# Optimization experiments

Hardware: AMD Instinct MI355X
Metric: run time of the kernel (lower is better)

## Reference

```python
import jax, jax.numpy as jnp
from jax import lax
import numpy as np

BLANK = 0
PAD = 1
LABEL_SMOOTHING = 0.1
CE_SCALE = 1.0
TEMPERATURE = 1.0

B, T, U1, D, V = 8, 128, 33, 512, 4096  # U1 = U + 1


def setup_inputs() -> dict:
    key = jax.random.key(0)
    k0, k1, k2, k3, k4 = jax.random.split(key, 5)
    x = jax.random.normal(k0, (B, T, U1, D), dtype=jnp.float32)
    weight = jax.random.normal(k1, (V, D), dtype=jnp.float32) * 0.02
    bias = jnp.zeros((V,), dtype=jnp.float32)
    src_lengths = jax.random.randint(k2, (B,), T // 2, T + 1, dtype=jnp.int32)
    tgt_lengths = jax.random.randint(k3, (B,), U1 // 2, U1, dtype=jnp.int32)
    targets = jax.random.randint(k4, (B, U1 - 1), 2, V, dtype=jnp.int32)
    pos = jnp.arange(U1 - 1, dtype=jnp.int32)
    targets = jnp.where(pos[None, :] < tgt_lengths[:, None], targets, PAD)
    return {'x': x, 'weight': weight, 'bias': bias, 'targets': targets,
            'src_lengths': src_lengths, 'tgt_lengths': tgt_lengths}


def _rnnt_neglogp(blank_lp, emit_lp, src_lengths, tgt_lengths):
    """RNN-T forward DP. blank_lp: (B,T,U1) log P(blank); emit_lp: (B,T,U) log P(y_u).
    Returns per-utterance negative log-likelihood, shape (B,)."""
    Bn, Tn, U1n = blank_lp.shape
    # alpha at t=0: can only emit labels -> prefix-sum of emit log-probs
    alpha0 = jnp.concatenate(
        [jnp.zeros((Bn, 1), blank_lp.dtype), jnp.cumsum(emit_lp[:, 0, :], axis=1)], axis=1)

    def t_step(alpha_prev, xs):
        blank_prev, emit_t = xs  # (B,U1), (B,U)
        a = alpha_prev + blank_prev  # blank transition from t-1
        def u_step(c, xu):
            a_u, e_prev = xu  # each (B,)
            c = jnp.logaddexp(a_u, c + e_prev)  # emit transition from u-1 at same t
            return c, c
        _, rest = lax.scan(u_step, a[:, 0], (a[:, 1:].T, emit_t.T))  # rest: (U,B)
        alpha_t = jnp.concatenate([a[:, :1], rest.T], axis=1)
        return alpha_t, alpha_t

    xs = (jnp.swapaxes(blank_lp[:, :-1], 0, 1), jnp.swapaxes(emit_lp[:, 1:], 0, 1))
    _, alphas_rest = lax.scan(t_step, alpha0, xs)  # (T-1,B,U1)
    alphas = jnp.concatenate([alpha0[None], alphas_rest], axis=0)  # (T,B,U1)
    bidx = jnp.arange(Bn)
    alpha_last_t = alphas[src_lengths - 1, bidx]  # (B,U1)
    a_fin = jnp.take_along_axis(alpha_last_t, tgt_lengths[:, None], axis=1)[:, 0]
    b_fin = blank_lp[bidx, src_lengths - 1, tgt_lengths]  # final blank emission
    return -(a_fin + b_fin)


def reference(x, weight, bias, targets, src_lengths, tgt_lengths):
    Vn = weight.shape[0]
    # joint logits over full lattice: (B,T,U1,V)
    logits = (jnp.einsum('btud,vd->btuv', x, weight) + bias).astype(jnp.float32)
    lp = jax.nn.log_softmax(logits / TEMPERATURE, axis=-1)
    blank_lp = lp[..., BLANK]  # (B,T,U1)
    emit_lp = jnp.take_along_axis(lp[:, :, :-1, :], targets[:, None, :, None].astype(jnp.int32), axis=3)[..., 0]  # (B,T,U)
    loss_prob = jnp.sum(_rnnt_neglogp(blank_lp, emit_lp, src_lengths, tgt_lengths))
    loss_delay = jnp.zeros((), jnp.float32)  # delay_func == 'zero'
    # label-smoothed CE on last valid encoder frame
    last_h = jnp.take_along_axis(x, (src_lengths - 1)[:, None, None, None], axis=1)[:, 0]  # (B,U1,D)
    last_h = last_h[:, :-1]  # (B,U,D)
    ce_logits = (jnp.einsum('bud,vd->buv', last_h, weight) + bias).astype(jnp.float32)
    lprobs = jax.nn.log_softmax(ce_logits, axis=-1)
    nll = -jnp.take_along_axis(lprobs, targets[..., None], axis=-1)[..., 0]  # (B,U)
    smooth = -jnp.sum(lprobs, axis=-1)
    mask = (targets != PAD).astype(lprobs.dtype)
    eps_i = LABEL_SMOOTHING / (Vn - 1)
    loss_smoothed = jnp.sum(((1.0 - LABEL_SMOOTHING - eps_i) * nll + eps_i * smooth) * mask)
    total = loss_prob + loss_delay + CE_SCALE * loss_smoothed
    return total
```

## Files before the change

kernel.cpp:

```cpp
#include <hip/hip_runtime.h>
#include <hip/hip_bf16.h>
#include <math.h>
#include <stdint.h>

#define B_ 8
#define T_ 128
#define U1_ 33
#define D_ 512
#define V_ 4096
#define M_ (B_*T_*U1_)

#define BLANK_ 0
#define PAD_ 1

#define TM 128
#define TN 128
#define BKB 128
#define NK (D_/BKB)
#define GN (V_/TN)

typedef __attribute__((ext_vector_type(4))) float fvec4;
typedef __attribute__((ext_vector_type(8))) int   i8v;
typedef __attribute__((ext_vector_type(4))) int   i4v;

#define SCALE_A 0x7F7F7F7Fu
#define SCALE_B 0x79797979u

__device__ __forceinline__ void load_lds16(const uint8_t* g, uint8_t* l) {
    __builtin_amdgcn_global_load_lds(
        (const __attribute__((address_space(1))) unsigned int*)g,
        (__attribute__((address_space(3))) unsigned int*)l, 16, 0, 0);
}

__device__ __forceinline__ unsigned pack4_fp8(fvec4 v) {
    int r = __builtin_amdgcn_cvt_pk_fp8_f32(v.x, v.y, 0, false);
    r = __builtin_amdgcn_cvt_pk_fp8_f32(v.z, v.w, r, true);
    return (unsigned)r;
}

__global__ void convert_kernel(const float* __restrict__ x, const float* __restrict__ w,
                               uint8_t* __restrict__ xf8, uint8_t* __restrict__ wf8)
{
    int i = blockIdx.x * 256 + threadIdx.x;
    int stride = gridDim.x * 256;
    const int nx = (M_ * D_) / 16;
    const int nw = (V_ * D_) / 16;
    for (int j = i; j < nx; j += stride) {
        const fvec4* p = (const fvec4*)x + (size_t)j * 4;
        uint4 o = { pack4_fp8(p[0]), pack4_fp8(p[1]), pack4_fp8(p[2]), pack4_fp8(p[3]) };
        ((uint4*)xf8)[j] = o;
    }
    for (int j = i; j < nw; j += stride) {
        const fvec4* p = (const fvec4*)w + (size_t)j * 4;
        fvec4 v0 = p[0]*64.0f, v1 = p[1]*64.0f, v2 = p[2]*64.0f, v3 = p[3]*64.0f;
        uint4 o = { pack4_fp8(v0), pack4_fp8(v1), pack4_fp8(v2), pack4_fp8(v3) };
        ((uint4*)wf8)[j] = o;
    }
}

__global__ void wsum_kernel(const float* __restrict__ w, const float* __restrict__ bias,
                            float* __restrict__ wsum)
{
    const int t = threadIdx.x;
    const int v0 = blockIdx.x * 128;
    float s0 = 0.0f, s1 = 0.0f;
    for (int v = 0; v < 128; v++) {
        s0 += w[(size_t)(v0 + v) * D_ + t];
        s1 += w[(size_t)(v0 + v) * D_ + t + 256];
    }
    atomicAdd(&wsum[t], s0);
    atomicAdd(&wsum[t + 256], s1);
    if (blockIdx.x == 0) {
        float b = 0.0f;
        for (int v = t; v < V_; v += 256) b += bias[v];
        atomicAdd(&wsum[D_], b);
    }
}

__global__ __launch_bounds__(256, 2)
void gemm_fused(const uint8_t* __restrict__ xf8, const uint8_t* __restrict__ wf8,
                const float* __restrict__ bias, const int* __restrict__ targets,
                float* __restrict__ partial_e,
                float* __restrict__ blank_z, float* __restrict__ emit_z)
{
    __shared__ __align__(16) uint8_t As[2][TM * BKB];
    __shared__ __align__(16) uint8_t Bs[2][TN * BKB];
    __shared__ float ps[TM];
    __shared__ int tgt_s[TM];

    const int tid  = threadIdx.x;
    const int lane = tid & 63;
    const int wid  = tid >> 6;
    const int m0   = blockIdx.x * TM;
    const int n0   = blockIdx.y * TN;

    const int srow = wid * 32 + (lane >> 3);
    const int schk = (lane & 7) ^ ((lane >> 3) & 7);
    const uint8_t* agp = xf8 + (size_t)(m0 + srow) * D_ + schk * 16;
    const uint8_t* bgp = wf8 + (size_t)(n0 + srow) * D_ + schk * 16;

    fvec4 acc[4][4];
#pragma unroll
    for (int i = 0; i < 4; i++)
#pragma unroll
        for (int j = 0; j < 4; j++) acc[i][j] = (fvec4)0.0f;

    const int wrow = (wid >> 1) * 64;
    const int wcol = (wid & 1) * 64;
    const int m15  = lane & 15;
    const int quad = lane >> 4;

    auto stage = [&](int buf, int ks) {
        const uint8_t* ag = agp + ks * BKB;
        const uint8_t* bg = bgp + ks * BKB;
#pragma unroll
        for (int j = 0; j < 4; j++) {
            load_lds16(ag + j * 8 * D_, &As[buf][(wid * 32 + j * 8) * BKB]);
            load_lds16(bg + j * 8 * D_, &Bs[buf][(wid * 32 + j * 8) * BKB]);
        }
    };

    stage(0, 0);
    if (tid < TM) {
        ps[tid] = 0.0f;
        int row = m0 + tid;
        int u = row % U1_;
        int b = row / (T_ * U1_);
        tgt_s[tid] = (u < U1_ - 1) ? targets[b * (U1_ - 1) + u] : -1;
    }
    __syncthreads();

    const int e   = m15 & 7;
    const int c0b = (((quad << 1) ^ e) << 4);

    for (int ks = 0; ks < NK; ks++) {
        const int cur = ks & 1;
        if (ks + 1 < NK) {
            stage(cur ^ 1, ks + 1);
            asm volatile("s_waitcnt vmcnt(8)" ::: "memory");
        } else {
            asm volatile("s_waitcnt vmcnt(0)" ::: "memory");
        }
        __builtin_amdgcn_s_barrier();

        i8v fa[4], fb[4];
#pragma unroll
        for (int mi = 0; mi < 4; mi++) {
            int base = (wrow + mi * 16 + m15) << 7;
            union { i4v h[2]; i8v w; } u;
            u.h[0] = *(const i4v*)&As[cur][base + c0b];
            u.h[1] = *(const i4v*)&As[cur][base + (c0b ^ 16)];
            fa[mi] = u.w;
        }
#pragma unroll
        for (int ni = 0; ni < 4; ni++) {
            int base = (wcol + ni * 16 + m15) << 7;
            union { i4v h[2]; i8v w; } u;
            u.h[0] = *(const i4v*)&Bs[cur][base + c0b];
            u.h[1] = *(const i4v*)&Bs[cur][base + (c0b ^ 16)];
            fb[ni] = u.w;
        }
#pragma unroll
        for (int mi = 0; mi < 4; mi++)
#pragma unroll
            for (int ni = 0; ni < 4; ni++)
                acc[mi][ni] = __builtin_amdgcn_mfma_scale_f32_16x16x128_f8f6f4(
                                  fa[mi], fb[ni], acc[mi][ni],
                                  0, 0,
                                  0, SCALE_A, 0, SCALE_B);
        __builtin_amdgcn_s_barrier();
    }

    float bv[4];
#pragma unroll
    for (int ni = 0; ni < 4; ni++) bv[ni] = bias[n0 + wcol + ni * 16 + m15];

    const bool blank_lane = (blockIdx.y == 0) && (wcol == 0) && (m15 == 0);

#pragma unroll
    for (int mi = 0; mi < 4; mi++) {
#pragma unroll
        for (int r = 0; r < 4; r++) {
            const int irow = wrow + mi * 16 + quad * 4 + r;
            float se = 0.0f;
#pragma unroll
            for (int ni = 0; ni < 4; ni++) {
                float z = acc[mi][ni][r] + bv[ni];
                se += __expf(z);
                int c = n0 + wcol + ni * 16 + m15;
                if (tgt_s[irow] == c) emit_z[m0 + irow] = z;
            }
            if (blank_lane) blank_z[m0 + irow] = acc[mi][0][r] + bv[0];
            se += __shfl_xor(se, 1, 64);
            se += __shfl_xor(se, 2, 64);
            se += __shfl_xor(se, 4, 64);
            se += __shfl_xor(se, 8, 64);
            if (m15 == 0) atomicAdd(&ps[irow], se);
        }
    }
    __syncthreads();
    if (tid < TM) {
        partial_e[(size_t)blockIdx.y * M_ + m0 + tid] = ps[tid];
    }
}

__global__ void lse_combine(const float* __restrict__ partial_e,
                            const float* __restrict__ emit_z, const int* __restrict__ targets,
                            const int* __restrict__ src_lengths,
                            const float* __restrict__ x, const float* __restrict__ wsum,
                            float* __restrict__ lse, float* __restrict__ out)
{
    int r = blockIdx.x * 256 + threadIdx.x;
    float se = 0.0f;
#pragma unroll
    for (int j = 0; j < GN; j++) se += partial_e[(size_t)j * M_ + r];
    float l = __logf(se);
    lse[r] = l;

    int b   = r / (T_ * U1_);
    int rem = r % (T_ * U1_);
    int t   = rem / U1_;
    int u   = rem % U1_;
    if (u < U1_ - 1 && t == src_lengths[b] - 1) {
        int tgt = targets[b * (U1_ - 1) + u];
        if (tgt != PAD_) {
            float sz = wsum[D_];
            const fvec4* xr = (const fvec4*)(x + (size_t)r * D_);
            const fvec4* ws = (const fvec4*)wsum;
#pragma unroll 4
            for (int d = 0; d < D_ / 4; d++) {
                fvec4 a = xr[d], wv = ws[d];
                sz += a.x * wv.x + a.y * wv.y + a.z * wv.z + a.w * wv.w;
            }
            float nll    = l - emit_z[r];
            float smooth = (float)V_ * l - sz;
            const float eps_i = 0.1f / (float)(V_ - 1);
            atomicAdd(out, (1.0f - 0.1f - eps_i) * nll + eps_i * smooth);
        }
    }
}

__global__ __launch_bounds__(256)
void dp_kernel(const float* __restrict__ blank_z, const float* __restrict__ emit_z,
               const float* __restrict__ lse, const int* __restrict__ src_lengths,
               const int* __restrict__ tgt_lengths, float* __restrict__ out)
{
    __shared__ float blp[T_ * U1_];
    __shared__ float elp[T_ * U1_];
    const int tid = threadIdx.x;
    const int b = blockIdx.x;
    for (int i = tid; i < T_ * U1_; i += 256) {
        int g = b * T_ * U1_ + i;
        float l = lse[g];
        blp[i] = blank_z[g] - l;
        elp[i] = emit_z[g] - l;
    }
    __syncthreads();
    if (tid >= 64) return;

    const int u = tid;
    const int ua = (u < U1_) ? u : U1_ - 1;
    const int sl = src_lengths[b], tl = tgt_lengths[b];

    float val = 0.0f;
    float afin = 0.0f;

    for (int d = 1; d <= (T_ - 1) + (U1_ - 1); d++) {
        int t = d - u;
        int tb = t - 1; tb = tb < 0 ? 0 : (tb > T_ - 1 ? T_ - 1 : tb);
        int tc = t < 0 ? 0 : (t > T_ - 1 ? T_ - 1 : t);
        float blv = blp[tb * U1_ + ua];
        float elv = elp[tc * U1_ + (ua > 0 ? ua - 1 : 0)];
        float up = __shfl_up(val, 1, 64);
        bool valid = (u < U1_) && (t >= 0) && (t < T_);
        if (valid) {
            if (t == 0) {
                val = up + elv;
            } else if (u == 0) {
                val = val + blv;
            } else {
                float a1 = val + blv;
                float a2 = up + elv;
                float mx = fmaxf(a1, a2), mn = fminf(a1, a2);
                val = mx + log1pf(__expf(mn - mx));
            }
            if (t == sl - 1 && u == tl) afin = val;
        }
    }
#pragma unroll
    for (int off = 1; off < 64; off <<= 1) afin += __shfl_xor(afin, off, 64);
    if (u == 0) {
        float bfin = blp[(sl - 1) * U1_ + tl];
        atomicAdd(out, -(afin + bfin));
    }
}

extern "C" void kernel_launch(void* const* d_in, const int* in_sizes, int n_in,
                              void* d_out, int out_size, void* d_ws, size_t ws_size,
                              hipStream_t stream)
{
    const float* x           = (const float*)d_in[0];
    const float* w           = (const float*)d_in[1];
    const float* bias        = (const float*)d_in[2];
    const int*   targets     = (const int*)d_in[3];
    const int*   src_lengths = (const int*)d_in[4];
    const int*   tgt_lengths = (const int*)d_in[5];
    float* out = (float*)d_out;

    char* p = (char*)d_ws;
    uint8_t* xf8 = (uint8_t*)p;     p += (size_t)M_ * D_;
    uint8_t* wf8 = (uint8_t*)p;     p += (size_t)V_ * D_;
    float* partial_e = (float*)p;   p += (size_t)GN * M_ * sizeof(float);
    float* lse       = (float*)p;   p += (size_t)M_ * sizeof(float);
    float* blank_z   = (float*)p;   p += (size_t)M_ * sizeof(float);
    float* emit_z    = (float*)p;   p += (size_t)M_ * sizeof(float);
    float* wsum      = (float*)p;   p += (size_t)(D_ + 4) * sizeof(float);

    hipMemsetAsync(out, 0, sizeof(float), stream);
    hipMemsetAsync(wsum, 0, (D_ + 4) * sizeof(float), stream);

    convert_kernel<<<1536, 256, 0, stream>>>(x, w, xf8, wf8);
    wsum_kernel<<<32, 256, 0, stream>>>(w, bias, wsum);
    gemm_fused<<<dim3(M_/TM, V_/TN), 256, 0, stream>>>(xf8, wf8, bias, targets,
                                                       partial_e, blank_z, emit_z);
    lse_combine<<<M_/256, 256, 0, stream>>>(partial_e, emit_z, targets,
                                            src_lengths, x, wsum, lse, out);
    dp_kernel<<<B_, 256, 0, stream>>>(blank_z, emit_z, lse, src_lengths, tgt_lengths, out);
}
```

Measured before the change: 451.9 us.

## Fuse wsum into convert, merge LSE combine into DP, swizzle GEMM tiles by XCD

The separate weight-sum kernel is folded into the conversion kernel. The LSE reduction and the label-smoothed CE term move into the DP kernel, which drops a launch and the lse buffer. The GEMM maps blocks to tiles grouped per XCD for better L2 locality, and the K loop now synchronises with __syncthreads instead of manual vmcnt waits. The risk is that the DP kernel runs only 8 blocks, so reducing all 32 partial sums per row there may be slow and latency-bound.

```diff
diff --git a/kernel.cpp b/kernel.cpp
--- a/kernel.cpp
+++ b/kernel.cpp
@@ -39,7 +39,9 @@
 }
 
 __global__ void convert_kernel(const float* __restrict__ x, const float* __restrict__ w,
-                               uint8_t* __restrict__ xf8, uint8_t* __restrict__ wf8)
+                               const float* __restrict__ bias,
+                               uint8_t* __restrict__ xf8, uint8_t* __restrict__ wf8,
+                               float* __restrict__ wsum)
 {
     int i = blockIdx.x * 256 + threadIdx.x;
     int stride = gridDim.x * 256;
@@ -56,24 +58,21 @@
         uint4 o = { pack4_fp8(v0), pack4_fp8(v1), pack4_fp8(v2), pack4_fp8(v3) };
         ((uint4*)wf8)[j] = o;
     }
-}
-
-__global__ void wsum_kernel(const float* __restrict__ w, const float* __restrict__ bias,
-                            float* __restrict__ wsum)
-{
-    const int t = threadIdx.x;
-    const int v0 = blockIdx.x * 128;
-    float s0 = 0.0f, s1 = 0.0f;
-    for (int v = 0; v < 128; v++) {
-        s0 += w[(size_t)(v0 + v) * D_ + t];
-        s1 += w[(size_t)(v0 + v) * D_ + t + 256];
-    }
-    atomicAdd(&wsum[t], s0);
-    atomicAdd(&wsum[t + 256], s1);
-    if (blockIdx.x == 0) {
-        float b = 0.0f;
-        for (int v = t; v < V_; v += 256) b += bias[v];
-        atomicAdd(&wsum[D_], b);
+    if (blockIdx.x < 32) {
+        const int t = threadIdx.x;
+        const int v0 = blockIdx.x * 128;
+        float s0 = 0.0f, s1 = 0.0f;
+        for (int v = 0; v < 128; v++) {
+            s0 += w[(size_t)(v0 + v) * D_ + t];
+            s1 += w[(size_t)(v0 + v) * D_ + t + 256];
+        }
+        atomicAdd(&wsum[t], s0);
+        atomicAdd(&wsum[t + 256], s1);
+        if (blockIdx.x == 0) {
+            float bsum = 0.0f;
+            for (int v = t; v < V_; v += 256) bsum += bias[v];
+            atomicAdd(&wsum[D_], bsum);
+        }
     }
 }
 
@@ -91,8 +90,14 @@
     const int tid  = threadIdx.x;
     const int lane = tid & 63;
     const int wid  = tid >> 6;
-    const int m0   = blockIdx.x * TM;
-    const int n0   = blockIdx.y * TN;
+
+    const int fid = blockIdx.y * gridDim.x + blockIdx.x;
+    const int xcd = fid & 7;
+    const int idx = fid >> 3;
+    const int mt  = xcd * 33 + (idx >> 5);
+    const int nt  = idx & 31;
+    const int m0  = mt * TM;
+    const int n0  = nt * TN;
 
     const int srow = wid * 32 + (lane >> 3);
     const int schk = (lane & 7) ^ ((lane >> 3) & 7);
@@ -121,6 +126,43 @@
     };
 
     stage(0, 0);
+    __syncthreads();
+
+    const int e   = m15 & 7;
+    const int c0b = (((quad << 1) ^ e) << 4);
+
+    for (int ks = 0; ks < NK; ks++) {
+        const int cur = ks & 1;
+        if (ks + 1 < NK) stage(cur ^ 1, ks + 1);
+
+        i8v fa[4], fb[4];
+#pragma unroll
+        for (int mi = 0; mi < 4; mi++) {
+            int base = (wrow + mi * 16 + m15) << 7;
+            union { i4v h[2]; i8v w; } u;
+            u.h[0] = *(const i4v*)&As[cur][base + c0b];
+            u.h[1] = *(const i4v*)&As[cur][base + (c0b ^ 16)];
+            fa[mi] = u.w;
+        }
+#pragma unroll
+        for (int ni = 0; ni < 4; ni++) {
+            int base = (wcol + ni * 16 + m15) << 7;
+            union { i4v h[2]; i8v w; } u;
+            u.h[0] = *(const i4v*)&Bs[cur][base + c0b];
+            u.h[1] = *(const i4v*)&Bs[cur][base + (c0b ^ 16)];
+            fb[ni] = u.w;
+        }
+#pragma unroll
+        for (int mi = 0; mi < 4; mi++)
+#pragma unroll
+            for (int ni = 0; ni < 4; ni++)
+                acc[mi][ni] = __builtin_amdgcn_mfma_scale_f32_16x16x128_f8f6f4(
+                                  fa[mi], fb[ni], acc[mi][ni],
+                                  0, 0,
+                                  0, SCALE_A, 0, SCALE_B);
+        __syncthreads();
+    }
+
     if (tid < TM) {
         ps[tid] = 0.0f;
         int row = m0 + tid;
@@ -130,52 +172,11 @@
     }
     __syncthreads();
 
-    const int e   = m15 & 7;
-    const int c0b = (((quad << 1) ^ e) << 4);
-
-    for (int ks = 0; ks < NK; ks++) {
-        const int cur = ks & 1;
-        if (ks + 1 < NK) {
-            stage(cur ^ 1, ks + 1);
-            asm volatile("s_waitcnt vmcnt(8)" ::: "memory");
-        } else {
-            asm volatile("s_waitcnt vmcnt(0)" ::: "memory");
-        }
-        __builtin_amdgcn_s_barrier();
-
-        i8v fa[4], fb[4];
-#pragma unroll
-        for (int mi = 0; mi < 4; mi++) {
-            int base = (wrow + mi * 16 + m15) << 7;
-            union { i4v h[2]; i8v w; } u;
-            u.h[0] = *(const i4v*)&As[cur][base + c0b];
-            u.h[1] = *(const i4v*)&As[cur][base + (c0b ^ 16)];
-            fa[mi] = u.w;
-        }
-#pragma unroll
-        for (int ni = 0; ni < 4; ni++) {
-            int base = (wcol + ni * 16 + m15) << 7;
-            union { i4v h[2]; i8v w; } u;
-            u.h[0] = *(const i4v*)&Bs[cur][base + c0b];
-            u.h[1] = *(const i4v*)&Bs[cur][base + (c0b ^ 16)];
-            fb[ni] = u.w;
-        }
-#pragma unroll
-        for (int mi = 0; mi < 4; mi++)
-#pragma unroll
-            for (int ni = 0; ni < 4; ni++)
-                acc[mi][ni] = __builtin_amdgcn_mfma_scale_f32_16x16x128_f8f6f4(
-                                  fa[mi], fb[ni], acc[mi][ni],
-                                  0, 0,
-                                  0, SCALE_A, 0, SCALE_B);
-        __builtin_amdgcn_s_barrier();
-    }
-
     float bv[4];
 #pragma unroll
     for (int ni = 0; ni < 4; ni++) bv[ni] = bias[n0 + wcol + ni * 16 + m15];
 
-    const bool blank_lane = (blockIdx.y == 0) && (wcol == 0) && (m15 == 0);
+    const bool blank_lane = (nt == 0) && (wcol == 0) && (m15 == 0);
 
 #pragma unroll
     for (int mi = 0; mi < 4; mi++) {
@@ -200,67 +201,65 @@
     }
     __syncthreads();
     if (tid < TM) {
-        partial_e[(size_t)blockIdx.y * M_ + m0 + tid] = ps[tid];
-    }
-}
-
-__global__ void lse_combine(const float* __restrict__ partial_e,
-                            const float* __restrict__ emit_z, const int* __restrict__ targets,
-                            const int* __restrict__ src_lengths,
-                            const float* __restrict__ x, const float* __restrict__ wsum,
-                            float* __restrict__ lse, float* __restrict__ out)
-{
-    int r = blockIdx.x * 256 + threadIdx.x;
-    float se = 0.0f;
-#pragma unroll
-    for (int j = 0; j < GN; j++) se += partial_e[(size_t)j * M_ + r];
-    float l = __logf(se);
-    lse[r] = l;
-
-    int b   = r / (T_ * U1_);
-    int rem = r % (T_ * U1_);
-    int t   = rem / U1_;
-    int u   = rem % U1_;
-    if (u < U1_ - 1 && t == src_lengths[b] - 1) {
-        int tgt = targets[b * (U1_ - 1) + u];
-        if (tgt != PAD_) {
-            float sz = wsum[D_];
-            const fvec4* xr = (const fvec4*)(x + (size_t)r * D_);
-            const fvec4* ws = (const fvec4*)wsum;
-#pragma unroll 4
-            for (int d = 0; d < D_ / 4; d++) {
-                fvec4 a = xr[d], wv = ws[d];
-                sz += a.x * wv.x + a.y * wv.y + a.z * wv.z + a.w * wv.w;
-            }
-            float nll    = l - emit_z[r];
-            float smooth = (float)V_ * l - sz;
-            const float eps_i = 0.1f / (float)(V_ - 1);
-            atomicAdd(out, (1.0f - 0.1f - eps_i) * nll + eps_i * smooth);
-        }
+        partial_e[(size_t)nt * M_ + m0 + tid] = ps[tid];
     }
 }
 
 __global__ __launch_bounds__(256)
-void dp_kernel(const float* __restrict__ blank_z, const float* __restrict__ emit_z,
-               const float* __restrict__ lse, const int* __restrict__ src_lengths,
-               const int* __restrict__ tgt_lengths, float* __restrict__ out)
+void dp_kernel(const float* __restrict__ partial_e,
+               const float* __restrict__ blank_z, const float* __restrict__ emit_z,
+               const int* __restrict__ targets,
+               const int* __restrict__ src_lengths, const int* __restrict__ tgt_lengths,
+               const float* __restrict__ x, const float* __restrict__ wsum,
+               float* __restrict__ out)
 {
     __shared__ float blp[T_ * U1_];
     __shared__ float elp[T_ * U1_];
     const int tid = threadIdx.x;
     const int b = blockIdx.x;
+    const int sl = src_lengths[b], tl = tgt_lengths[b];
+
     for (int i = tid; i < T_ * U1_; i += 256) {
         int g = b * T_ * U1_ + i;
-        float l = lse[g];
+        float se = 0.0f;
+#pragma unroll
+        for (int j = 0; j < GN; j++) se += partial_e[(size_t)j * M_ + g];
+        float l = __logf(se);
         blp[i] = blank_z[g] - l;
         elp[i] = emit_z[g] - l;
     }
     __syncthreads();
-    if (tid >= 64) return;
+
+    if (tid >= 64) {
+        if (tid < 64 + (U1_ - 1)) {
+            int u = tid - 64;
+            int tgt = targets[b * (U1_ - 1) + u];
+            if (tgt != PAD_) {
+                int i = (sl - 1) * U1_ + u;
+                int g = b * T_ * U1_ + i;
+                float se = 0.0f;
+#pragma unroll
+                for (int j = 0; j < GN; j++) se += partial_e[(size_t)j * M_ + g];
+                float l = __logf(se);
+                float sz = wsum[D_];
+                const fvec4* xr = (const fvec4*)(x + (size_t)g * D_);
+                const fvec4* ws = (const fvec4*)wsum;
+#pragma unroll 4
+                for (int d = 0; d < D_ / 4; d++) {
+                    fvec4 a = xr[d], wv = ws[d];
+                    sz += a.x * wv.x + a.y * wv.y + a.z * wv.z + a.w * wv.w;
+                }
+                float nll    = l - emit_z[g];
+                float smooth = (float)V_ * l - sz;
+                const float eps_i = 0.1f / (float)(V_ - 1);
+                atomicAdd(out, (1.0f - 0.1f - eps_i) * nll + eps_i * smooth);
+            }
+        }
+        return;
+    }
 
     const int u = tid;
     const int ua = (u < U1_) ? u : U1_ - 1;
-    const int sl = src_lengths[b], tl = tgt_lengths[b];
 
     float val = 0.0f;
     float afin = 0.0f;
@@ -311,7 +310,6 @@
     uint8_t* xf8 = (uint8_t*)p;     p += (size_t)M_ * D_;
     uint8_t* wf8 = (uint8_t*)p;     p += (size_t)V_ * D_;
     float* partial_e = (float*)p;   p += (size_t)GN * M_ * sizeof(float);
-    float* lse       = (float*)p;   p += (size_t)M_ * sizeof(float);
     float* blank_z   = (float*)p;   p += (size_t)M_ * sizeof(float);
     float* emit_z    = (float*)p;   p += (size_t)M_ * sizeof(float);
     float* wsum      = (float*)p;   p += (size_t)(D_ + 4) * sizeof(float);
@@ -319,11 +317,9 @@
     hipMemsetAsync(out, 0, sizeof(float), stream);
     hipMemsetAsync(wsum, 0, (D_ + 4) * sizeof(float), stream);
 
-    convert_kernel<<<1536, 256, 0, stream>>>(x, w, xf8, wf8);
-    wsum_kernel<<<32, 256, 0, stream>>>(w, bias, wsum);
+    convert_kernel<<<1536, 256, 0, stream>>>(x, w, bias, xf8, wf8, wsum);
     gemm_fused<<<dim3(M_/TM, V_/TN), 256, 0, stream>>>(xf8, wf8, bias, targets,
                                                        partial_e, blank_z, emit_z);
-    lse_combine<<<M_/256, 256, 0, stream>>>(partial_e, emit_z, targets,
-                                            src_lengths, x, wsum, lse, out);
-    dp_kernel<<<B_, 256, 0, stream>>>(blank_z, emit_z, lse, src_lengths, tgt_lengths, out);
-}
+    dp_kernel<<<B_, 256, 0, stream>>>(partial_e, blank_z, emit_z, targets,
+                                      src_lengths, tgt_lengths, x, wsum, out);
+}
```

Result: faster. 418.6 us (-7.4%).

## Fuse wsum into convert kernel, remap GEMM tiles per XCD, simplify k-loop sync

Applied to the files above, without the earlier changes.

Folds the weight column-sum kernel into the fp8 conversion kernel, saving one launch. Remaps GEMM block indices so each XCD (fid&7) works on a contiguous band of 33 M-tiles across all 32 N-tiles, aiming for better L2 reuse of the A rows. Moves the target/ps setup after the main loop and replaces the manual vmcnt waits with plain __syncthreads. The plain barriers may leave the async global_load_lds prefetch less well overlapped with compute, or unsynchronised if the compiler does not insert a vmcnt wait before the barrier.

```diff
diff --git a/kernel.cpp b/kernel.cpp
--- a/kernel.cpp
+++ b/kernel.cpp
@@ -39,7 +39,9 @@
 }
 
 __global__ void convert_kernel(const float* __restrict__ x, const float* __restrict__ w,
-                               uint8_t* __restrict__ xf8, uint8_t* __restrict__ wf8)
+                               const float* __restrict__ bias,
+                               uint8_t* __restrict__ xf8, uint8_t* __restrict__ wf8,
+                               float* __restrict__ wsum)
 {
     int i = blockIdx.x * 256 + threadIdx.x;
     int stride = gridDim.x * 256;
@@ -56,24 +58,21 @@
         uint4 o = { pack4_fp8(v0), pack4_fp8(v1), pack4_fp8(v2), pack4_fp8(v3) };
         ((uint4*)wf8)[j] = o;
     }
-}
-
-__global__ void wsum_kernel(const float* __restrict__ w, const float* __restrict__ bias,
-                            float* __restrict__ wsum)
-{
-    const int t = threadIdx.x;
-    const int v0 = blockIdx.x * 128;
-    float s0 = 0.0f, s1 = 0.0f;
-    for (int v = 0; v < 128; v++) {
-        s0 += w[(size_t)(v0 + v) * D_ + t];
-        s1 += w[(size_t)(v0 + v) * D_ + t + 256];
-    }
-    atomicAdd(&wsum[t], s0);
-    atomicAdd(&wsum[t + 256], s1);
-    if (blockIdx.x == 0) {
-        float b = 0.0f;
-        for (int v = t; v < V_; v += 256) b += bias[v];
-        atomicAdd(&wsum[D_], b);
+    if (blockIdx.x < 32) {
+        const int t = threadIdx.x;
+        const int v0 = blockIdx.x * 128;
+        float s0 = 0.0f, s1 = 0.0f;
+        for (int v = 0; v < 128; v++) {
+            s0 += w[(size_t)(v0 + v) * D_ + t];
+            s1 += w[(size_t)(v0 + v) * D_ + t + 256];
+        }
+        atomicAdd(&wsum[t], s0);
+        atomicAdd(&wsum[t + 256], s1);
+        if (blockIdx.x == 0) {
+            float bsum = 0.0f;
+            for (int v = t; v < V_; v += 256) bsum += bias[v];
+            atomicAdd(&wsum[D_], bsum);
+        }
     }
 }
 
@@ -91,8 +90,14 @@
     const int tid  = threadIdx.x;
     const int lane = tid & 63;
     const int wid  = tid >> 6;
-    const int m0   = blockIdx.x * TM;
-    const int n0   = blockIdx.y * TN;
+
+    const int fid = blockIdx.y * gridDim.x + blockIdx.x;
+    const int xcd = fid & 7;
+    const int idx = fid >> 3;
+    const int mt  = xcd * 33 + (idx >> 5);
+    const int nt  = idx & 31;
+    const int m0  = mt * TM;
+    const int n0  = nt * TN;
 
     const int srow = wid * 32 + (lane >> 3);
     const int schk = (lane & 7) ^ ((lane >> 3) & 7);
@@ -121,6 +126,43 @@
     };
 
     stage(0, 0);
+    __syncthreads();
+
+    const int e   = m15 & 7;
+    const int c0b = (((quad << 1) ^ e) << 4);
+
+    for (int ks = 0; ks < NK; ks++) {
+        const int cur = ks & 1;
+        if (ks + 1 < NK) stage(cur ^ 1, ks + 1);
+
+        i8v fa[4], fb[4];
+#pragma unroll
+        for (int mi = 0; mi < 4; mi++) {
+            int base = (wrow + mi * 16 + m15) << 7;
+            union { i4v h[2]; i8v w; } u;
+            u.h[0] = *(const i4v*)&As[cur][base + c0b];
+            u.h[1] = *(const i4v*)&As[cur][base + (c0b ^ 16)];
+            fa[mi] = u.w;
+        }
+#pragma unroll
+        for (int ni = 0; ni < 4; ni++) {
+            int base = (wcol + ni * 16 + m15) << 7;
+            union { i4v h[2]; i8v w; } u;
+            u.h[0] = *(const i4v*)&Bs[cur][base + c0b];
+            u.h[1] = *(const i4v*)&Bs[cur][base + (c0b ^ 16)];
+            fb[ni] = u.w;
+        }
+#pragma unroll
+        for (int mi = 0; mi < 4; mi++)
+#pragma unroll
+            for (int ni = 0; ni < 4; ni++)
+                acc[mi][ni] = __builtin_amdgcn_mfma_scale_f32_16x16x128_f8f6f4(
+                                  fa[mi], fb[ni], acc[mi][ni],
+                                  0, 0,
+                                  0, SCALE_A, 0, SCALE_B);
+        __syncthreads();
+    }
+
     if (tid < TM) {
         ps[tid] = 0.0f;
         int row = m0 + tid;
@@ -130,52 +172,11 @@
     }
     __syncthreads();
 
-    const int e   = m15 & 7;
-    const int c0b = (((quad << 1) ^ e) << 4);
-
-    for (int ks = 0; ks < NK; ks++) {
-        const int cur = ks & 1;
-        if (ks + 1 < NK) {
-            stage(cur ^ 1, ks + 1);
-            asm volatile("s_waitcnt vmcnt(8)" ::: "memory");
-        } else {
-            asm volatile("s_waitcnt vmcnt(0)" ::: "memory");
-        }
-        __builtin_amdgcn_s_barrier();
-
-        i8v fa[4], fb[4];
-#pragma unroll
-        for (int mi = 0; mi < 4; mi++) {
-            int base = (wrow + mi * 16 + m15) << 7;
-            union { i4v h[2]; i8v w; } u;
-            u.h[0] = *(const i4v*)&As[cur][base + c0b];
-            u.h[1] = *(const i4v*)&As[cur][base + (c0b ^ 16)];
-            fa[mi] = u.w;
-        }
-#pragma unroll
-        for (int ni = 0; ni < 4; ni++) {
-            int base = (wcol + ni * 16 + m15) << 7;
-            union { i4v h[2]; i8v w; } u;
-            u.h[0] = *(const i4v*)&Bs[cur][base + c0b];
-            u.h[1] = *(const i4v*)&Bs[cur][base + (c0b ^ 16)];
-            fb[ni] = u.w;
-        }
-#pragma unroll
-        for (int mi = 0; mi < 4; mi++)
-#pragma unroll
-            for (int ni = 0; ni < 4; ni++)
-                acc[mi][ni] = __builtin_amdgcn_mfma_scale_f32_16x16x128_f8f6f4(
-                                  fa[mi], fb[ni], acc[mi][ni],
-                                  0, 0,
-                                  0, SCALE_A, 0, SCALE_B);
-        __builtin_amdgcn_s_barrier();
-    }
-
     float bv[4];
 #pragma unroll
     for (int ni = 0; ni < 4; ni++) bv[ni] = bias[n0 + wcol + ni * 16 + m15];
 
-    const bool blank_lane = (blockIdx.y == 0) && (wcol == 0) && (m15 == 0);
+    const bool blank_lane = (nt == 0) && (wcol == 0) && (m15 == 0);
 
 #pragma unroll
     for (int mi = 0; mi < 4; mi++) {
@@ -200,7 +201,7 @@
     }
     __syncthreads();
     if (tid < TM) {
-        partial_e[(size_t)blockIdx.y * M_ + m0 + tid] = ps[tid];
+        partial_e[(size_t)nt * M_ + m0 + tid] = ps[tid];
     }
 }
 
@@ -319,8 +320,7 @@
     hipMemsetAsync(out, 0, sizeof(float), stream);
     hipMemsetAsync(wsum, 0, (D_ + 4) * sizeof(float), stream);
 
-    convert_kernel<<<1536, 256, 0, stream>>>(x, w, xf8, wf8);
-    wsum_kernel<<<32, 256, 0, stream>>>(w, bias, wsum);
+    convert_kernel<<<1536, 256, 0, stream>>>(x, w, bias, xf8, wf8, wsum);
     gemm_fused<<<dim3(M_/TM, V_/TN), 256, 0, stream>>>(xf8, wf8, bias, targets,
                                                        partial_e, blank_z, emit_z);
     lse_combine<<<M_/256, 256, 0, stream>>>(partial_e, emit_z, targets,
```

Result: faster. 366.9 us (-18.8%).
